# Optimization experiments

Hardware: AMD Instinct MI355X
Metric: run time of the kernel (lower is better)

## Reference

```python
import jax, jax.numpy as jnp
import numpy as np
from jax import lax

PATCH = 16  # get_patch patch_size; crop taken deterministically at (0,0) (original uses random offsets)
K = 5       # predicted kernel size (kernel_v.view(b,5,5))


def setup_inputs() -> dict:
    key = jax.random.key(0)
    ks = jax.random.split(key, 6)
    B, Cf, H, W = 16, 32, 64, 64
    Ci, Hi, Wi = 3, 512, 512
    return {
        "feature": jax.random.normal(ks[0], (B, Cf, H, W), dtype=jnp.float32),
        "img": jax.random.normal(ks[1], (B, Ci, Hi, Wi), dtype=jnp.float32),
        "conv_w": jax.random.normal(ks[2], (16, 32, 16, 16), dtype=jnp.float32) * 0.02,
        "conv_b": jax.random.normal(ks[3], (16,), dtype=jnp.float32) * 0.02,
        "lin_w": jax.random.normal(ks[4], (25, 144), dtype=jnp.float32) * 0.05,
        "lin_b": jax.random.normal(ks[5], (25,), dtype=jnp.float32) * 0.05,
    }


def reference(feature, img, conv_w, conv_b, lin_w, lin_b):
    B, C, H, W = img.shape
    # --- kernel predictor (eval mode: dropout is identity) ---
    patch = feature[:, :, :PATCH, :PATCH]  # deterministic top-left 16x16 crop
    f = lax.conv_general_dilated(
        patch, conv_w, window_strides=(1, 1), padding=[(1, 1), (1, 1)],
        dimension_numbers=("NCHW", "OIHW", "NCHW"))
    f = f + conv_b[None, :, None, None]            # [B,16,3,3]
    f = f.reshape(B, -1)                           # flatten -> [B,144]
    f = jax.nn.gelu(f, approximate=False)          # torch GELU default = exact erf
    kernel_v = f @ lin_w.T + lin_b                 # [B,25]
    # --- per-sample 5x5 filtering (kornia.filter2D: reflect pad, correlation,
    #     same kernel broadcast over channels) fused as one grouped depthwise conv ---
    k = jnp.broadcast_to(kernel_v.reshape(B, 1, K, K), (B, C, K, K)).reshape(B * C, 1, K, K)
    pad = K // 2
    xp = jnp.pad(img, ((0, 0), (0, 0), (pad, pad), (pad, pad)), mode="reflect")
    xp = xp.reshape(1, B * C, H + 2 * pad, W + 2 * pad)
    out = lax.conv_general_dilated(
        xp, k, window_strides=(1, 1), padding="VALID",
        feature_group_count=B * C,
        dimension_numbers=("NCHW", "OIHW", "NCHW"))
    return out.reshape(B, C, H, W)
```

## Files before the change

kernel.cpp:

```cpp
#include <hip/hip_runtime.h>
#include <math.h>


#define B_  16
#define C_  3
#define H_  512
#define W_  512

__global__ __launch_bounds__(256) void patch_conv_kernel(
    const float* __restrict__ feature,
    const float* __restrict__ conv_w,
    const float* __restrict__ conv_b,
    float* __restrict__ g_out)
{
    __shared__ float patch_raw[17 + 8192 + 17];
    __shared__ float red[9][4];
    float* patch = patch_raw + 17;

    int blk = blockIdx.x;
    int b   = blk >> 4;
    int oc  = blk & 15;
    int tid = threadIdx.x;

    const float* fb = feature + (size_t)b * 32 * 4096;
    const float* wb = conv_w + (size_t)oc * 8192;

    if (tid < 17) { patch_raw[tid] = 0.f; patch_raw[17 + 8192 + tid] = 0.f; }

    for (int i = tid; i < 8192; i += 256) {
        int ic = i >> 8;
        int r  = i & 255;
        patch[i] = fb[ic * 4096 + (r >> 4) * 64 + (r & 15)];
    }

    float wreg[32];
    #pragma unroll
    for (int ic = 0; ic < 32; ic++) wreg[ic] = wb[ic * 256 + tid];

    __syncthreads();

    int kh = tid >> 4;
    int kw = tid & 15;

    float acc[9];
    #pragma unroll
    for (int k = 0; k < 9; k++) acc[k] = 0.f;

    #pragma unroll 4
    for (int ic = 0; ic < 32; ic++) {
        int base = ic * 256 + tid;
        float wv = wreg[ic];
        #pragma unroll
        for (int di = 0; di < 3; di++) {
            #pragma unroll
            for (int dj = 0; dj < 3; dj++) {
                acc[di * 3 + dj] += patch[base + (di - 1) * 16 + (dj - 1)] * wv;
            }
        }
    }

    #pragma unroll
    for (int di = 0; di < 3; di++) {
        #pragma unroll
        for (int dj = 0; dj < 3; dj++) {
            bool ok = ((unsigned)(kh + di - 1) < 16u) &&
                      ((unsigned)(kw + dj - 1) < 16u);
            if (!ok) acc[di * 3 + dj] = 0.f;
        }
    }

    #pragma unroll
    for (int k = 0; k < 9; k++) {
        float v = acc[k];
        #pragma unroll
        for (int off = 32; off > 0; off >>= 1)
            v += __shfl_xor(v, off, 64);
        acc[k] = v;
    }
    int wid  = tid >> 6;
    int lane = tid & 63;
    if (lane == 0) {
        #pragma unroll
        for (int k = 0; k < 9; k++) red[k][wid] = acc[k];
    }
    __syncthreads();
    if (tid < 9) {
        float s = red[tid][0] + red[tid][1] + red[tid][2] + red[tid][3];
        s += conv_b[oc];
        float g = 0.5f * s * (1.0f + erff(s * 0.70710678118654752f));
        g_out[(b * 16 + oc) * 9 + tid] = g;
    }
}

__global__ __launch_bounds__(256) void kv_kernel(
    const float* __restrict__ g_in,
    const float* __restrict__ lin_w,
    const float* __restrict__ lin_b,
    float* __restrict__ kv_out)
{
    __shared__ float wsh[25 * 144];
    __shared__ float gsh[144];
    int b   = blockIdx.x;
    int tid = threadIdx.x;

    for (int i = tid; i < 25 * 144; i += 256) wsh[i] = lin_w[i];
    if (tid < 144) gsh[tid] = g_in[b * 144 + tid];
    __syncthreads();

    if (tid < 25) {
        float acc = lin_b[tid];
        #pragma unroll 8
        for (int j = 0; j < 144; j++) acc += gsh[j] * wsh[tid * 144 + j];
        kv_out[b * 25 + tid] = acc;
    }
}

#define TSX  64
#define TSY  128

__device__ __forceinline__ int reflect_idx(int v, int n) {
    v = (v < 0) ? -v : v;
    v = (v >= n) ? (2 * n - 2 - v) : v;
    return v;
}

template <bool XFAST>
__device__ __forceinline__ void dw_tile(
    const float* __restrict__ ip, float* __restrict__ op,
    const float* w, int ty0, int tx0, int tx, int tyl)
{
    int gx0 = tx0 + tx;
    int xid[8];
    if (!XFAST) {
        #pragma unroll
        for (int j = 0; j < 8; j++) xid[j] = reflect_idx(gx0 - 2 + j, W_);
    }

    float acc[8][4];
    #pragma unroll
    for (int i = 0; i < 8; i++)
        #pragma unroll
        for (int j = 0; j < 4; j++) acc[i][j] = 0.f;

    float win[4][8];

    #pragma unroll
    for (int r = 0; r < 4; r++) {
        int gy = reflect_idx(ty0 + tyl + r - 2, H_);
        const float* rowp = ip + (size_t)gy * W_;
        if (XFAST) {
            const float* rp = rowp + gx0;
            float2 a = *(const float2*)(rp - 2);
            float4 m = *(const float4*)(rp);
            float2 c = *(const float2*)(rp + 4);
            win[r][0] = a.x; win[r][1] = a.y;
            win[r][2] = m.x; win[r][3] = m.y; win[r][4] = m.z; win[r][5] = m.w;
            win[r][6] = c.x; win[r][7] = c.y;
        } else {
            #pragma unroll
            for (int j = 0; j < 8; j++) win[r][j] = rowp[xid[j]];
        }
    }

    #pragma unroll
    for (int r = 0; r < 12; r++) {
        const float* x = win[r & 3];
        #pragma unroll
        for (int orow = 0; orow < 8; orow++) {
            int dy = r - orow;
            if (dy >= 0 && dy < 5) {
                #pragma unroll
                for (int dx = 0; dx < 5; dx++) {
                    float wv = w[dy * 5 + dx];
                    #pragma unroll
                    for (int oc = 0; oc < 4; oc++)
                        acc[orow][oc] += wv * x[oc + dx];
                }
            }
        }
        if (r + 4 < 12) {
            int rn = r + 4;
            int gy = reflect_idx(ty0 + tyl + rn - 2, H_);
            const float* rowp = ip + (size_t)gy * W_;
            float* wdst = win[r & 3];
            if (XFAST) {
                const float* rp = rowp + gx0;
                float2 a = *(const float2*)(rp - 2);
                float4 m = *(const float4*)(rp);
                float2 c = *(const float2*)(rp + 4);
                wdst[0] = a.x; wdst[1] = a.y;
                wdst[2] = m.x; wdst[3] = m.y; wdst[4] = m.z; wdst[5] = m.w;
                wdst[6] = c.x; wdst[7] = c.y;
            } else {
                #pragma unroll
                for (int j = 0; j < 8; j++) wdst[j] = rowp[xid[j]];
            }
        }
    }

    #pragma unroll
    for (int orow = 0; orow < 8; orow++) {
        float4 o;
        o.x = acc[orow][0]; o.y = acc[orow][1];
        o.z = acc[orow][2]; o.w = acc[orow][3];
        *(float4*)&op[(size_t)(ty0 + tyl + orow) * W_ + gx0] = o;
    }
}

__global__ __launch_bounds__(256) void depthwise_kernel(
    const float* __restrict__ img,
    const float* __restrict__ kv,
    float* __restrict__ out)
{
    int bc   = blockIdx.y;
    int b    = bc / C_;
    int tile = blockIdx.x;
    int tyi  = tile >> 3;
    int txi  = tile & 7;
    int ty0  = tyi * TSY;
    int tx0  = txi * TSX;

    int tid = threadIdx.x;
    int tx  = (tid & 15) * 4;
    int tyl = (tid >> 4) * 8;

    float w[25];
    {
        const float* kvp = kv + b * 25;
        #pragma unroll
        for (int i = 0; i < 25; i++)
            w[i] = __int_as_float(
                __builtin_amdgcn_readfirstlane(__float_as_int(kvp[i])));
    }

    const float* ip = img + (size_t)bc * H_ * W_;
    float* op       = out + (size_t)bc * H_ * W_;

    if (txi >= 1 && txi <= 6)
        dw_tile<true >(ip, op, w, ty0, tx0, tx, tyl);
    else
        dw_tile<false>(ip, op, w, ty0, tx0, tx, tyl);
}

extern "C" void kernel_launch(void* const* d_in, const int* in_sizes, int n_in,
                              void* d_out, int out_size, void* d_ws, size_t ws_size,
                              hipStream_t stream) {
    const float* feature = (const float*)d_in[0];
    const float* img     = (const float*)d_in[1];
    const float* conv_w  = (const float*)d_in[2];
    const float* conv_b  = (const float*)d_in[3];
    const float* lin_w   = (const float*)d_in[4];
    const float* lin_b   = (const float*)d_in[5];
    float* out = (float*)d_out;

    float* g_ws  = (float*)d_ws;
    float* kv_ws = g_ws + 2304;

    patch_conv_kernel<<<B_ * 16, 256, 0, stream>>>(feature, conv_w, conv_b, g_ws);
    kv_kernel<<<B_, 256, 0, stream>>>(g_ws, lin_w, lin_b, kv_ws);

    dim3 grid(32, B_ * C_);
    depthwise_kernel<<<grid, 256, 0, stream>>>(img, kv_ws, out);
}
```

Baseline: 135.0 us.

## Fuse linear kernel-prediction layer into depthwise filter kernel

Removes the separate kv_kernel launch and has every depthwise block compute the 25 predicted filter weights from the GELU features itself, using 200 threads with shuffle reductions into LDS. The first image rows are loaded before this compute so their latency overlaps the small GEMV. This cuts one kernel launch and its serialization gap, at the cost of recomputing the tiny linear layer in every block and adding a block-wide barrier.

```diff
diff --git a/kernel.cpp b/kernel.cpp
--- a/kernel.cpp
+++ b/kernel.cpp
@@ -92,29 +92,6 @@
     }
 }
 
-__global__ __launch_bounds__(256) void kv_kernel(
-    const float* __restrict__ g_in,
-    const float* __restrict__ lin_w,
-    const float* __restrict__ lin_b,
-    float* __restrict__ kv_out)
-{
-    __shared__ float wsh[25 * 144];
-    __shared__ float gsh[144];
-    int b   = blockIdx.x;
-    int tid = threadIdx.x;
-
-    for (int i = tid; i < 25 * 144; i += 256) wsh[i] = lin_w[i];
-    if (tid < 144) gsh[tid] = g_in[b * 144 + tid];
-    __syncthreads();
-
-    if (tid < 25) {
-        float acc = lin_b[tid];
-        #pragma unroll 8
-        for (int j = 0; j < 144; j++) acc += gsh[j] * wsh[tid * 144 + j];
-        kv_out[b * 25 + tid] = acc;
-    }
-}
-
 #define TSX  64
 #define TSY  128
 
@@ -125,9 +102,13 @@
 }
 
 template <bool XFAST>
-__device__ __forceinline__ void dw_tile(
+__device__ __forceinline__ void dw_tile_fused(
     const float* __restrict__ ip, float* __restrict__ op,
-    const float* w, int ty0, int tx0, int tx, int tyl)
+    const float* __restrict__ gb,
+    const float* __restrict__ lin_w,
+    const float* __restrict__ lin_b,
+    float* __restrict__ kv_lds,
+    int ty0, int tx0, int tx, int tyl, int tid)
 {
     int gx0 = tx0 + tx;
     int xid[8];
@@ -135,12 +116,6 @@
         #pragma unroll
         for (int j = 0; j < 8; j++) xid[j] = reflect_idx(gx0 - 2 + j, W_);
     }
-
-    float acc[8][4];
-    #pragma unroll
-    for (int i = 0; i < 8; i++)
-        #pragma unroll
-        for (int j = 0; j < 4; j++) acc[i][j] = 0.f;
 
     float win[4][8];
 
@@ -161,6 +136,33 @@
             for (int j = 0; j < 8; j++) win[r][j] = rowp[xid[j]];
         }
     }
+
+    if (tid < 200) {
+        int k = tid >> 3;
+        int s = tid & 7;
+        const float* wr = lin_w + k * 144;
+        float p = 0.f;
+        #pragma unroll
+        for (int i = 0; i < 18; i++)
+            p += gb[s + 8 * i] * wr[s + 8 * i];
+        p += __shfl_xor(p, 1, 64);
+        p += __shfl_xor(p, 2, 64);
+        p += __shfl_xor(p, 4, 64);
+        if (s == 0) kv_lds[k] = p + lin_b[k];
+    }
+    __syncthreads();
+
+    float w[25];
+    #pragma unroll
+    for (int i = 0; i < 25; i++)
+        w[i] = __int_as_float(
+            __builtin_amdgcn_readfirstlane(__float_as_int(kv_lds[i])));
+
+    float acc[8][4];
+    #pragma unroll
+    for (int i = 0; i < 8; i++)
+        #pragma unroll
+        for (int j = 0; j < 4; j++) acc[i][j] = 0.f;
 
     #pragma unroll
     for (int r = 0; r < 12; r++) {
@@ -209,9 +211,13 @@
 
 __global__ __launch_bounds__(256) void depthwise_kernel(
     const float* __restrict__ img,
-    const float* __restrict__ kv,
+    const float* __restrict__ g,
+    const float* __restrict__ lin_w,
+    const float* __restrict__ lin_b,
     float* __restrict__ out)
 {
+    __shared__ float kv_lds[32];
+
     int bc   = blockIdx.y;
     int b    = bc / C_;
     int tile = blockIdx.x;
@@ -224,22 +230,16 @@
     int tx  = (tid & 15) * 4;
     int tyl = (tid >> 4) * 8;
 
-    float w[25];
-    {
-        const float* kvp = kv + b * 25;
-        #pragma unroll
-        for (int i = 0; i < 25; i++)
-            w[i] = __int_as_float(
-                __builtin_amdgcn_readfirstlane(__float_as_int(kvp[i])));
-    }
-
     const float* ip = img + (size_t)bc * H_ * W_;
     float* op       = out + (size_t)bc * H_ * W_;
+    const float* gb = g + b * 144;
 
     if (txi >= 1 && txi <= 6)
-        dw_tile<true >(ip, op, w, ty0, tx0, tx, tyl);
+        dw_tile_fused<true >(ip, op, gb, lin_w, lin_b, kv_lds,
+                             ty0, tx0, tx, tyl, tid);
     else
-        dw_tile<false>(ip, op, w, ty0, tx0, tx, tyl);
+        dw_tile_fused<false>(ip, op, gb, lin_w, lin_b, kv_lds,
+                             ty0, tx0, tx, tyl, tid);
 }
 
 extern "C" void kernel_launch(void* const* d_in, const int* in_sizes, int n_in,
@@ -253,12 +253,10 @@
     const float* lin_b   = (const float*)d_in[5];
     float* out = (float*)d_out;
 
-    float* g_ws  = (float*)d_ws;
-    float* kv_ws = g_ws + 2304;
+    float* g_ws = (float*)d_ws;
 
     patch_conv_kernel<<<B_ * 16, 256, 0, stream>>>(feature, conv_w, conv_b, g_ws);
-    kv_kernel<<<B_, 256, 0, stream>>>(g_ws, lin_w, lin_b, kv_ws);
 
     dim3 grid(32, B_ * C_);
-    depthwise_kernel<<<grid, 256, 0, stream>>>(img, kv_ws, out);
-}
+    depthwise_kernel<<<grid, 256, 0, stream>>>(img, g_ws, lin_w, lin_b, out);
+}
```

New measurement: 131.7 us. 2.5% less time.
